# Kernel tuning notes

Hardware: AMD Instinct MI355X
Metric: run time of the kernel (lower is better)

## Reference

```python
import jax, jax.numpy as jnp
import numpy as np

B, T, N, U = 16, 512, 2048, 64  # batch_size, dim1, dim2 (=nodes), units


def setup_inputs() -> dict:
    key = jax.random.key(0)
    k1, k2, k3, k4 = jax.random.split(key, 4)
    x = jax.random.normal(k1, (B, T, N), dtype=jnp.float32)
    Adj = jax.random.uniform(k2, (N, N), dtype=jnp.float32)
    W = jax.random.normal(k3, (U, N), dtype=jnp.float32) * 0.05  # 'uniform' init stand-in
    b = jax.random.normal(k4, (U,), dtype=jnp.float32) * 0.05
    return {"x": x, "Adj": Adj, "W": W, "b": b}


def reference(x, Adj, W, b):
    # Original loop: out_i[b,t,j] = sum_k x[b,t,k] * Adj[j,k] * W[i,k] + b[i],
    # then mean over i. By linearity this equals a single matmul with the
    # unit-averaged weight vector and the averaged bias.
    w_bar = jnp.mean(W, axis=0)              # [N]
    w_eff = Adj * w_bar                       # [N(j), N(k)] : Adj[j,k] * w_bar[k]
    out = jnp.einsum('btk,jk->btj', x, w_eff) + jnp.mean(b)
    return out  # [B, T, N]
```

## Files before the change

### kernel.cpp

```cpp
#include <hip/hip_runtime.h>

#define N_DIM 2048
#define U_DIM 64
#define M_DIM 8192
#define K_DIM 2048

typedef __bf16 bf16x8 __attribute__((ext_vector_type(8)));
typedef float  floatx4 __attribute__((ext_vector_type(4)));
typedef unsigned short ushort8 __attribute__((ext_vector_type(8)));

#define AS1 __attribute__((address_space(1)))
#define AS3 __attribute__((address_space(3)))

__device__ __forceinline__ unsigned short f_to_bf16_rne(float f) {
    unsigned int x;
    __builtin_memcpy(&x, &f, 4);
    x += 0x7fffu + ((x >> 16) & 1u);
    return (unsigned short)(x >> 16);
}

__global__ __launch_bounds__(256) void prep_kernel(
    const float* __restrict__ W,
    const float* __restrict__ b,
    float* __restrict__ wbar,
    float* __restrict__ bmean) {
    int k = blockIdx.x * 256 + threadIdx.x;
    float s = 0.f;
#pragma unroll
    for (int i = 0; i < U_DIM; ++i) s += W[i * N_DIM + k];
    wbar[k] = s * (1.f / U_DIM);

    if (blockIdx.x == 0 && threadIdx.x < 64) {
        float v = b[threadIdx.x];
#pragma unroll
        for (int off = 32; off > 0; off >>= 1) v += __shfl_down(v, off);
        if (threadIdx.x == 0) bmean[0] = v * (1.f / U_DIM);
    }
}

__global__ __launch_bounds__(256) void weff_kernel(
    const float* __restrict__ Adj,
    const float* __restrict__ wbar,
    unsigned short* __restrict__ weff) {
    long long idx = ((long long)blockIdx.x * 256 + threadIdx.x) * 8;
    int k = (int)(idx & (N_DIM - 1));
    floatx4 a0 = *(const floatx4*)(Adj + idx);
    floatx4 a1 = *(const floatx4*)(Adj + idx + 4);
    floatx4 w0 = *(const floatx4*)(wbar + k);
    floatx4 w1 = *(const floatx4*)(wbar + k + 4);
    ushort8 ov;
#pragma unroll
    for (int j = 0; j < 4; ++j) {
        ov[j]     = f_to_bf16_rne(a0[j] * w0[j]);
        ov[j + 4] = f_to_bf16_rne(a1[j] * w1[j]);
    }
    *(ushort8*)(weff + idx) = ov;
}

__global__ __launch_bounds__(256) void convx_kernel(
    const float* __restrict__ x,
    unsigned short* __restrict__ xbf) {
    long long idx = ((long long)blockIdx.x * 256 + threadIdx.x) * 8;
    floatx4 a0 = *(const floatx4*)(x + idx);
    floatx4 a1 = *(const floatx4*)(x + idx + 4);
    ushort8 ov;
#pragma unroll
    for (int j = 0; j < 4; ++j) {
        ov[j]     = f_to_bf16_rne(a0[j]);
        ov[j + 4] = f_to_bf16_rne(a1[j]);
    }
    *(ushort8*)(xbf + idx) = ov;
}

#define BM 128
#define BN 128
#define BK 32

__global__ __launch_bounds__(256) void gemm_bt_kernel(
    const unsigned short* __restrict__ A,
    const unsigned short* __restrict__ Bt,
    const float* __restrict__ bmeanp,
    float* __restrict__ C) {
    __shared__ __align__(16) unsigned short sA[BM * BK];
    __shared__ __align__(16) unsigned short sB[BN * BK];

    const int tid  = threadIdx.x;
    const int w    = tid >> 6;
    const int lane = tid & 63;
    const int tile_m = blockIdx.y * BM;
    const int tile_n = blockIdx.x * BN;

    const float bmean = bmeanp[0];

    const int srow = lane >> 2;
    const int scol = (lane & 3) * 8;
    const unsigned short* gA0 = A + (size_t)(tile_m + (w * 2 + 0) * 16 + srow) * K_DIM + scol;
    const unsigned short* gA1 = A + (size_t)(tile_m + (w * 2 + 1) * 16 + srow) * K_DIM + scol;
    const unsigned short* gB0 = Bt + (size_t)(tile_n + (w * 2 + 0) * 16 + srow) * K_DIM + scol;
    const unsigned short* gB1 = Bt + (size_t)(tile_n + (w * 2 + 1) * 16 + srow) * K_DIM + scol;
    unsigned short* lA0 = &sA[(w * 2 + 0) * 16 * BK];
    unsigned short* lA1 = &sA[(w * 2 + 1) * 16 * BK];
    unsigned short* lB0 = &sB[(w * 2 + 0) * 16 * BK];
    unsigned short* lB1 = &sB[(w * 2 + 1) * 16 * BK];

    const int wrow = (w >> 1) * 64;
    const int wcol = (w & 1) * 64;
    const int fr = lane & 15;
    const int fq = lane >> 4;
    int aoff[4], boff[4];
#pragma unroll
    for (int i = 0; i < 4; ++i) {
        aoff[i] = (wrow + i * 16 + fr) * BK + fq * 8;
        boff[i] = (wcol + i * 16 + fr) * BK + fq * 8;
    }

    floatx4 acc[4][4];
#pragma unroll
    for (int mi = 0; mi < 4; ++mi)
#pragma unroll
        for (int ni = 0; ni < 4; ++ni) acc[mi][ni] = (floatx4){0.f, 0.f, 0.f, 0.f};

    for (int k0 = 0; k0 < K_DIM; k0 += BK) {
        __syncthreads();
        __builtin_amdgcn_global_load_lds((const AS1 void*)(gA0 + k0), (AS3 void*)lA0, 16, 0, 0);
        __builtin_amdgcn_global_load_lds((const AS1 void*)(gA1 + k0), (AS3 void*)lA1, 16, 0, 0);
        __builtin_amdgcn_global_load_lds((const AS1 void*)(gB0 + k0), (AS3 void*)lB0, 16, 0, 0);
        __builtin_amdgcn_global_load_lds((const AS1 void*)(gB1 + k0), (AS3 void*)lB1, 16, 0, 0);
        __syncthreads();

        bf16x8 af[4], bf[4];
#pragma unroll
        for (int i = 0; i < 4; ++i) {
            af[i] = *(const bf16x8*)&sA[aoff[i]];
            bf[i] = *(const bf16x8*)&sB[boff[i]];
        }
#pragma unroll
        for (int mi = 0; mi < 4; ++mi)
#pragma unroll
            for (int ni = 0; ni < 4; ++ni)
                acc[mi][ni] = __builtin_amdgcn_mfma_f32_16x16x32_bf16(
                    af[mi], bf[ni], acc[mi][ni], 0, 0, 0);
    }

    const int crow = tile_m + wrow + fq * 4;
    const int ccol = tile_n + wcol + fr;
#pragma unroll
    for (int mi = 0; mi < 4; ++mi)
#pragma unroll
        for (int ni = 0; ni < 4; ++ni)
#pragma unroll
            for (int r = 0; r < 4; ++r) {
                int gm = crow + mi * 16 + r;
                int gn = ccol + ni * 16;
                C[(size_t)gm * N_DIM + gn] = acc[mi][ni][r] + bmean;
            }
}

extern "C" void kernel_launch(void* const* d_in, const int* in_sizes, int n_in,
                              void* d_out, int out_size, void* d_ws, size_t ws_size,
                              hipStream_t stream) {
    (void)in_sizes; (void)n_in; (void)out_size;
    const float* x   = (const float*)d_in[0];
    const float* Adj = (const float*)d_in[1];
    const float* W   = (const float*)d_in[2];
    const float* b   = (const float*)d_in[3];
    float* out = (float*)d_out;

    char* ws = (char*)d_ws;
    float* wbar  = (float*)ws;
    float* bmean = (float*)(ws + 8192);
    unsigned short* weff = (unsigned short*)(ws + 16384);
    const size_t weff_bytes = (size_t)N_DIM * N_DIM * 2;
    const size_t xbf_off = 16384 + weff_bytes;
    unsigned short* xbf = (unsigned short*)(ws + xbf_off);

    size_t avail = (ws_size > xbf_off) ? (ws_size - xbf_off) : 0;
    long long max_rows = (long long)(avail / ((size_t)K_DIM * 2)) / BM * BM;
    if (max_rows < BM) max_rows = BM;
    if (max_rows > M_DIM) max_rows = M_DIM;

    prep_kernel<<<N_DIM / 256, 256, 0, stream>>>(W, b, wbar, bmean);
    weff_kernel<<<(int)(((size_t)N_DIM * N_DIM / 8) / 256), 256, 0, stream>>>(Adj, wbar, weff);

    for (long long m0 = 0; m0 < M_DIM; m0 += max_rows) {
        long long rows = (M_DIM - m0 < max_rows) ? (M_DIM - m0) : max_rows;
        convx_kernel<<<(int)rows, 256, 0, stream>>>(x + m0 * K_DIM, xbf);
        dim3 grid(N_DIM / BN, (int)(rows / BM));
        gemm_bt_kernel<<<grid, 256, 0, stream>>>(xbf, weff, bmean, out + m0 * (size_t)N_DIM);
    }
}
```

Measured before the change: 249.1 us.

## Switch GEMM to 32x32x16 MFMA and XOR-swizzle LDS tile layout

Replaces the sixteen 16x16x32 bf16 MFMAs per wave with eight 32x32x16 MFMAs over two K-halves per BK step, and remaps the accumulator epilogue to match. It also XOR-swizzles the 16-byte chunk column within each LDS row on both the global-to-LDS load and the fragment reads, to reduce LDS bank conflicts. The larger MFMA needs fewer LDS fragment loads per FLOP. The cost is a different output write pattern and extra index arithmetic, and the swizzle mapping must exactly match between writer and reader.

```diff
diff --git a/kernel.cpp b/kernel.cpp
--- a/kernel.cpp
+++ b/kernel.cpp
@@ -6,7 +6,8 @@
 #define K_DIM 2048
 
 typedef __bf16 bf16x8 __attribute__((ext_vector_type(8)));
-typedef float  floatx4 __attribute__((ext_vector_type(4)));
+typedef float  floatx4  __attribute__((ext_vector_type(4)));
+typedef float  floatx16 __attribute__((ext_vector_type(16)));
 typedef unsigned short ushort8 __attribute__((ext_vector_type(8)));
 
 #define AS1 __attribute__((address_space(1)))
@@ -20,10 +21,8 @@
 }
 
 __global__ __launch_bounds__(256) void prep_kernel(
-    const float* __restrict__ W,
-    const float* __restrict__ b,
-    float* __restrict__ wbar,
-    float* __restrict__ bmean) {
+    const float* __restrict__ W, const float* __restrict__ b,
+    float* __restrict__ wbar, float* __restrict__ bmean) {
     int k = blockIdx.x * 256 + threadIdx.x;
     float s = 0.f;
 #pragma unroll
@@ -39,8 +38,7 @@
 }
 
 __global__ __launch_bounds__(256) void weff_kernel(
-    const float* __restrict__ Adj,
-    const float* __restrict__ wbar,
+    const float* __restrict__ Adj, const float* __restrict__ wbar,
     unsigned short* __restrict__ weff) {
     long long idx = ((long long)blockIdx.x * 256 + threadIdx.x) * 8;
     int k = (int)(idx & (N_DIM - 1));
@@ -58,8 +56,7 @@
 }
 
 __global__ __launch_bounds__(256) void convx_kernel(
-    const float* __restrict__ x,
-    unsigned short* __restrict__ xbf) {
+    const float* __restrict__ x, unsigned short* __restrict__ xbf) {
     long long idx = ((long long)blockIdx.x * 256 + threadIdx.x) * 8;
     floatx4 a0 = *(const floatx4*)(x + idx);
     floatx4 a1 = *(const floatx4*)(x + idx + 4);
@@ -93,7 +90,8 @@
     const float bmean = bmeanp[0];
 
     const int srow = lane >> 2;
-    const int scol = (lane & 3) * 8;
+    const int skc  = (lane & 3) ^ ((lane >> 3) & 3);
+    const int scol = skc * 8;
     const unsigned short* gA0 = A + (size_t)(tile_m + (w * 2 + 0) * 16 + srow) * K_DIM + scol;
     const unsigned short* gA1 = A + (size_t)(tile_m + (w * 2 + 1) * 16 + srow) * K_DIM + scol;
     const unsigned short* gB0 = Bt + (size_t)(tile_n + (w * 2 + 0) * 16 + srow) * K_DIM + scol;
@@ -105,20 +103,28 @@
 
     const int wrow = (w >> 1) * 64;
     const int wcol = (w & 1) * 64;
-    const int fr = lane & 15;
-    const int fq = lane >> 4;
-    int aoff[4], boff[4];
-#pragma unroll
-    for (int i = 0; i < 4; ++i) {
-        aoff[i] = (wrow + i * 16 + fr) * BK + fq * 8;
-        boff[i] = (wcol + i * 16 + fr) * BK + fq * 8;
-    }
-
-    floatx4 acc[4][4];
-#pragma unroll
-    for (int mi = 0; mi < 4; ++mi)
-#pragma unroll
-        for (int ni = 0; ni < 4; ++ni) acc[mi][ni] = (floatx4){0.f, 0.f, 0.f, 0.f};
+    const int fr = lane & 31;
+    const int fh = lane >> 5;
+    int aoff[2][2], boff[2][2];
+#pragma unroll
+    for (int ti = 0; ti < 2; ++ti) {
+#pragma unroll
+        for (int s = 0; s < 2; ++s) {
+            int ra = wrow + ti * 32 + fr;
+            int rb = wcol + ti * 32 + fr;
+            int kc = fh + 2 * s;
+            aoff[ti][s] = ra * BK + ((kc ^ ((ra >> 1) & 3)) * 8);
+            boff[ti][s] = rb * BK + ((kc ^ ((rb >> 1) & 3)) * 8);
+        }
+    }
+
+    floatx16 acc[2][2];
+#pragma unroll
+    for (int tm = 0; tm < 2; ++tm)
+#pragma unroll
+        for (int tn = 0; tn < 2; ++tn)
+#pragma unroll
+            for (int r = 0; r < 16; ++r) acc[tm][tn][r] = 0.f;
 
     for (int k0 = 0; k0 < K_DIM; k0 += BK) {
         __syncthreads();
@@ -128,31 +134,34 @@
         __builtin_amdgcn_global_load_lds((const AS1 void*)(gB1 + k0), (AS3 void*)lB1, 16, 0, 0);
         __syncthreads();
 
-        bf16x8 af[4], bf[4];
-#pragma unroll
-        for (int i = 0; i < 4; ++i) {
-            af[i] = *(const bf16x8*)&sA[aoff[i]];
-            bf[i] = *(const bf16x8*)&sB[boff[i]];
-        }
-#pragma unroll
-        for (int mi = 0; mi < 4; ++mi)
-#pragma unroll
-            for (int ni = 0; ni < 4; ++ni)
-                acc[mi][ni] = __builtin_amdgcn_mfma_f32_16x16x32_bf16(
-                    af[mi], bf[ni], acc[mi][ni], 0, 0, 0);
-    }
-
-    const int crow = tile_m + wrow + fq * 4;
-    const int ccol = tile_n + wcol + fr;
-#pragma unroll
-    for (int mi = 0; mi < 4; ++mi)
-#pragma unroll
-        for (int ni = 0; ni < 4; ++ni)
-#pragma unroll
-            for (int r = 0; r < 4; ++r) {
-                int gm = crow + mi * 16 + r;
-                int gn = ccol + ni * 16;
-                C[(size_t)gm * N_DIM + gn] = acc[mi][ni][r] + bmean;
+        bf16x8 af[2][2], bf[2][2];
+#pragma unroll
+        for (int ti = 0; ti < 2; ++ti)
+#pragma unroll
+            for (int s = 0; s < 2; ++s) {
+                af[ti][s] = *(const bf16x8*)&sA[aoff[ti][s]];
+                bf[ti][s] = *(const bf16x8*)&sB[boff[ti][s]];
+            }
+#pragma unroll
+        for (int s = 0; s < 2; ++s)
+#pragma unroll
+            for (int tm = 0; tm < 2; ++tm)
+#pragma unroll
+                for (int tn = 0; tn < 2; ++tn)
+                    acc[tm][tn] = __builtin_amdgcn_mfma_f32_32x32x16_bf16(
+                        af[tm][s], bf[tn][s], acc[tm][tn], 0, 0, 0);
+    }
+
+#pragma unroll
+    for (int tm = 0; tm < 2; ++tm)
+#pragma unroll
+        for (int tn = 0; tn < 2; ++tn)
+#pragma unroll
+            for (int r = 0; r < 16; ++r) {
+                int row = (r & 3) + 8 * (r >> 2) + 4 * fh;
+                int gm = tile_m + wrow + tm * 32 + row;
+                int gn = tile_n + wcol + tn * 32 + fr;
+                C[(size_t)gm * N_DIM + gn] = acc[tm][tn][r] + bmean;
             }
 }
 
```

After: 250.7 us. Within noise of the previous version (+0.7%).

## Double GEMM K-tile to 64 and XOR-swizzle LDS layout

Applied to the files above, without the earlier changes.

Raises the GEMM K-tile from 32 to 64, which halves the number of barrier-separated load/compute iterations and doubles the MFMA work per sync. It also applies an XOR swizzle to the 16-byte chunk positions, both when global_load_lds writes into LDS and when fragments are read back, to spread ds_read traffic across LDS banks. The cost is twice the LDS footprint per block and more address registers, which may reduce occupancy. There is still no double buffering, so loads and MFMAs do not overlap.

```diff
diff --git a/kernel.cpp b/kernel.cpp
--- a/kernel.cpp
+++ b/kernel.cpp
@@ -20,10 +20,8 @@
 }
 
 __global__ __launch_bounds__(256) void prep_kernel(
-    const float* __restrict__ W,
-    const float* __restrict__ b,
-    float* __restrict__ wbar,
-    float* __restrict__ bmean) {
+    const float* __restrict__ W, const float* __restrict__ b,
+    float* __restrict__ wbar, float* __restrict__ bmean) {
     int k = blockIdx.x * 256 + threadIdx.x;
     float s = 0.f;
 #pragma unroll
@@ -39,8 +37,7 @@
 }
 
 __global__ __launch_bounds__(256) void weff_kernel(
-    const float* __restrict__ Adj,
-    const float* __restrict__ wbar,
+    const float* __restrict__ Adj, const float* __restrict__ wbar,
     unsigned short* __restrict__ weff) {
     long long idx = ((long long)blockIdx.x * 256 + threadIdx.x) * 8;
     int k = (int)(idx & (N_DIM - 1));
@@ -58,8 +55,7 @@
 }
 
 __global__ __launch_bounds__(256) void convx_kernel(
-    const float* __restrict__ x,
-    unsigned short* __restrict__ xbf) {
+    const float* __restrict__ x, unsigned short* __restrict__ xbf) {
     long long idx = ((long long)blockIdx.x * 256 + threadIdx.x) * 8;
     floatx4 a0 = *(const floatx4*)(x + idx);
     floatx4 a1 = *(const floatx4*)(x + idx + 4);
@@ -74,7 +70,7 @@
 
 #define BM 128
 #define BN 128
-#define BK 32
+#define BK 64
 
 __global__ __launch_bounds__(256) void gemm_bt_kernel(
     const unsigned short* __restrict__ A,
@@ -92,27 +88,36 @@
 
     const float bmean = bmeanp[0];
 
-    const int srow = lane >> 2;
-    const int scol = (lane & 3) * 8;
-    const unsigned short* gA0 = A + (size_t)(tile_m + (w * 2 + 0) * 16 + srow) * K_DIM + scol;
-    const unsigned short* gA1 = A + (size_t)(tile_m + (w * 2 + 1) * 16 + srow) * K_DIM + scol;
-    const unsigned short* gB0 = Bt + (size_t)(tile_n + (w * 2 + 0) * 16 + srow) * K_DIM + scol;
-    const unsigned short* gB1 = Bt + (size_t)(tile_n + (w * 2 + 1) * 16 + srow) * K_DIM + scol;
-    unsigned short* lA0 = &sA[(w * 2 + 0) * 16 * BK];
-    unsigned short* lA1 = &sA[(w * 2 + 1) * 16 * BK];
-    unsigned short* lB0 = &sB[(w * 2 + 0) * 16 * BK];
-    unsigned short* lB1 = &sB[(w * 2 + 1) * 16 * BK];
+    const int srow_in = lane >> 3;
+    const int skc     = (lane & 7) ^ srow_in;
+    const int scol    = skc * 8;
+    const unsigned short* gA[4];
+    const unsigned short* gB[4];
+    unsigned short* lA[4];
+    unsigned short* lB[4];
+#pragma unroll
+    for (int i = 0; i < 4; ++i) {
+        int c = w * 4 + i;
+        gA[i] = A  + (size_t)(tile_m + c * 8 + srow_in) * K_DIM + scol;
+        gB[i] = Bt + (size_t)(tile_n + c * 8 + srow_in) * K_DIM + scol;
+        lA[i] = &sA[c * 8 * BK];
+        lB[i] = &sB[c * 8 * BK];
+    }
 
     const int wrow = (w >> 1) * 64;
     const int wcol = (w & 1) * 64;
     const int fr = lane & 15;
     const int fq = lane >> 4;
-    int aoff[4], boff[4];
-#pragma unroll
-    for (int i = 0; i < 4; ++i) {
-        aoff[i] = (wrow + i * 16 + fr) * BK + fq * 8;
-        boff[i] = (wcol + i * 16 + fr) * BK + fq * 8;
-    }
+    int aoff[4][2], boff[4][2];
+#pragma unroll
+    for (int i = 0; i < 4; ++i)
+#pragma unroll
+        for (int s = 0; s < 2; ++s) {
+            int kc = s * 4 + fq;
+            int slot = kc ^ (fr & 7);
+            aoff[i][s] = (wrow + i * 16 + fr) * BK + slot * 8;
+            boff[i][s] = (wcol + i * 16 + fr) * BK + slot * 8;
+        }
 
     floatx4 acc[4][4];
 #pragma unroll
@@ -122,24 +127,30 @@
 
     for (int k0 = 0; k0 < K_DIM; k0 += BK) {
         __syncthreads();
-        __builtin_amdgcn_global_load_lds((const AS1 void*)(gA0 + k0), (AS3 void*)lA0, 16, 0, 0);
-        __builtin_amdgcn_global_load_lds((const AS1 void*)(gA1 + k0), (AS3 void*)lA1, 16, 0, 0);
-        __builtin_amdgcn_global_load_lds((const AS1 void*)(gB0 + k0), (AS3 void*)lB0, 16, 0, 0);
-        __builtin_amdgcn_global_load_lds((const AS1 void*)(gB1 + k0), (AS3 void*)lB1, 16, 0, 0);
+#pragma unroll
+        for (int i = 0; i < 4; ++i) {
+            __builtin_amdgcn_global_load_lds((const AS1 void*)(gA[i] + k0),
+                                             (AS3 void*)lA[i], 16, 0, 0);
+            __builtin_amdgcn_global_load_lds((const AS1 void*)(gB[i] + k0),
+                                             (AS3 void*)lB[i], 16, 0, 0);
+        }
         __syncthreads();
 
-        bf16x8 af[4], bf[4];
-#pragma unroll
-        for (int i = 0; i < 4; ++i) {
-            af[i] = *(const bf16x8*)&sA[aoff[i]];
-            bf[i] = *(const bf16x8*)&sB[boff[i]];
+#pragma unroll
+        for (int s = 0; s < 2; ++s) {
+            bf16x8 af[4], bf[4];
+#pragma unroll
+            for (int i = 0; i < 4; ++i) {
+                af[i] = *(const bf16x8*)&sA[aoff[i][s]];
+                bf[i] = *(const bf16x8*)&sB[boff[i][s]];
+            }
+#pragma unroll
+            for (int mi = 0; mi < 4; ++mi)
+#pragma unroll
+                for (int ni = 0; ni < 4; ++ni)
+                    acc[mi][ni] = __builtin_amdgcn_mfma_f32_16x16x32_bf16(
+                        af[mi], bf[ni], acc[mi][ni], 0, 0, 0);
         }
-#pragma unroll
-        for (int mi = 0; mi < 4; ++mi)
-#pragma unroll
-            for (int ni = 0; ni < 4; ++ni)
-                acc[mi][ni] = __builtin_amdgcn_mfma_f32_16x16x32_bf16(
-                    af[mi], bf[ni], acc[mi][ni], 0, 0, 0);
     }
 
     const int crow = tile_m + wrow + fq * 4;
```

New measurement: 226.7 us. 9.0% less time.
